# Kernel optimization log

Measured on AMD Instinct MI355X. Metric: run time of the kernel, lower is better.

Reference implementation:

```python
import jax, jax.numpy as jnp
import numpy as np

DIM = 1024
HEADS = 16
DIM_HEAD = 64
DEPTH = 12
LN_EPS = 1e-5


def setup_inputs() -> dict:
    key = jax.random.key(0)
    k1, k2, k3 = jax.random.split(key, 3)
    B, N = 4, 2048
    inner = HEADS * DIM_HEAD
    x = jax.random.normal(k1, (B, N, DIM), dtype=jnp.float32)
    ln_w = jnp.ones((DIM,), jnp.float32)
    ln_b = jnp.zeros((DIM,), jnp.float32)
    w_qkv = jax.random.normal(k2, (DIM, 3 * inner), jnp.float32) * (DIM ** -0.5)
    w_out = jax.random.normal(k3, (inner, DIM), jnp.float32) * (inner ** -0.5)
    b_out = jnp.zeros((DIM,), jnp.float32)
    return {"x": x, "ln_w": ln_w, "ln_b": ln_b, "w_qkv": w_qkv,
            "w_out": w_out, "b_out": b_out, "layer_index": 2}


def reference(x, ln_w, ln_b, w_qkv, w_out, b_out, layer_index):
    B, N, D = x.shape
    scale = DIM_HEAD ** -0.5
    # LayerNorm
    mu = jnp.mean(x, axis=-1, keepdims=True)
    var = jnp.mean(jnp.square(x - mu), axis=-1, keepdims=True)
    xn = (x - mu) * jax.lax.rsqrt(var + LN_EPS) * ln_w + ln_b
    # QKV projection (no bias), split heads: b n (h d) -> b h n d
    qkv = xn @ w_qkv  # [B, N, 3*H*Dh]
    q, k, v = jnp.split(qkv, 3, axis=-1)
    def heads(t):
        return t.reshape(B, N, HEADS, DIM_HEAD).transpose(0, 2, 1, 3)
    q, k, v = heads(q), heads(k), heads(v)
    dots = jnp.einsum('bhnd,bhmd->bhnm', q, k) * scale  # [B,H,N,N]
    if layer_index < DEPTH // 2:
        attn = jax.nn.relu(dots)
    else:
        attn = jax.nn.softmax(dots, axis=-1)
    attn = attn / N  # divide by x.shape[1]
    out = jnp.einsum('bhnm,bhmd->bhnd', attn, v)
    out = out.transpose(0, 2, 1, 3).reshape(B, N, HEADS * DIM_HEAD)
    # to_out (heads > 1): Linear + (inactive) dropout
    return out @ w_out + b_out
```

## Files before the change

### kernel.cpp

```cpp
#include <hip/hip_runtime.h>
#include <stdint.h>

typedef __bf16 bf16x8 __attribute__((ext_vector_type(8)));
typedef __bf16 bf16x4 __attribute__((ext_vector_type(4)));
typedef float f32x4 __attribute__((ext_vector_type(4)));

#define PSCALE (0.125f / 2048.0f)

#define GLOAD16(src, dst)                                                      \
  __builtin_amdgcn_global_load_lds(                                            \
      (__attribute__((address_space(1))) void*)const_cast<__bf16*>(src),       \
      (__attribute__((address_space(3))) void*)(dst), 16, 0, 0)

__global__ __launch_bounds__(256) void ln_fused(const float* __restrict__ x,
                                                const float* __restrict__ w,
                                                const float* __restrict__ b,
                                                __bf16* __restrict__ xn) {
  const int row = blockIdx.x;
  const int t = threadIdx.x;
  const float4 v = ((const float4*)(x + (size_t)row * 1024))[t];
  float s = v.x + v.y + v.z + v.w;
  float ss = v.x * v.x + v.y * v.y + v.z * v.z + v.w * v.w;
#pragma unroll
  for (int o = 32; o; o >>= 1) {
    s += __shfl_down(s, o);
    ss += __shfl_down(ss, o);
  }
  __shared__ float red[8];
  if ((t & 63) == 0) {
    red[t >> 6] = s;
    red[4 + (t >> 6)] = ss;
  }
  __syncthreads();
  const float tot = red[0] + red[1] + red[2] + red[3];
  const float tot2 = red[4] + red[5] + red[6] + red[7];
  const float mu = tot * (1.0f / 1024.0f);
  const float var = tot2 * (1.0f / 1024.0f) - mu * mu;
  const float rs = rsqrtf(var + 1e-5f);
  const float4 wv = ((const float4*)w)[t];
  const float4 bv = ((const float4*)b)[t];
  bf16x4 o;
  o[0] = (__bf16)((v.x - mu) * rs * wv.x + bv.x);
  o[1] = (__bf16)((v.y - mu) * rs * wv.y + bv.y);
  o[2] = (__bf16)((v.z - mu) * rs * wv.z + bv.z);
  o[3] = (__bf16)((v.w - mu) * rs * wv.w + bv.w);
  ((bf16x4*)xn)[(size_t)row * 256 + t] = o;
}

__global__ __launch_bounds__(256) void transpose_cvt(const float* __restrict__ A,
                                                     __bf16* __restrict__ At,
                                                     int R, int C) {
  __shared__ __bf16 T[64][72];
  const int rb = blockIdx.y * 64, cb = blockIdx.x * 64;
  const int tid = threadIdx.x;
  const int r = tid >> 2, cg = tid & 3;
#pragma unroll
  for (int k = 0; k < 4; ++k) {
    const float4 v =
        *(const float4*)(A + (size_t)(rb + r) * C + cb + cg * 16 + k * 4);
    T[cg * 16 + k * 4 + 0][r] = (__bf16)v.x;
    T[cg * 16 + k * 4 + 1][r] = (__bf16)v.y;
    T[cg * 16 + k * 4 + 2][r] = (__bf16)v.z;
    T[cg * 16 + k * 4 + 3][r] = (__bf16)v.w;
  }
  __syncthreads();
#pragma unroll
  for (int i = 0; i < 2; ++i) {
    const int j = i * 256 + tid;
    const int c = j >> 3, s8 = j & 7;
    const bf16x8 o = *(const bf16x8*)&T[c][s8 * 8];
    *(bf16x8*)(At + (size_t)(cb + c) * R + rb + s8 * 8) = o;
  }
}

__device__ __forceinline__ void stage_128x64(const __bf16* __restrict__ g,
                                             int ld, __bf16* lds) {
  const int lane = threadIdx.x & 63, w = threadIdx.x >> 6;
#pragma unroll
  for (int i = 0; i < 4; ++i) {
    const int j = i * 256 + w * 64 + lane;
    const int row = j >> 3, slot = j & 7;
    const __bf16* src = g + (size_t)row * ld + ((slot ^ (row & 7)) << 3);
    GLOAD16(src, lds + (size_t)(i * 256 + w * 64) * 8);
  }
}

template <int MODE>
__global__ __launch_bounds__(256) void gemm_nt(
    const __bf16* __restrict__ A, const __bf16* __restrict__ B, int K,
    float* __restrict__ outF, __bf16* __restrict__ Qo, __bf16* __restrict__ Ko,
    __bf16* __restrict__ Vto, const float* __restrict__ bias) {
  __shared__ __bf16 As[128 * 64];
  __shared__ __bf16 Bs[128 * 64];
  const int lane = threadIdx.x & 63, w = threadIdx.x >> 6;
  const int rb = blockIdx.y * 128, cb = blockIdx.x * 128;
  const int wr = (w >> 1) * 64, wc = (w & 1) * 64;
  f32x4 acc[4][4] = {};
  const __bf16* Ab = A + (size_t)rb * K;
  const __bf16* Bb = B + (size_t)cb * K;
  const int nkb = K >> 6;
  for (int kb = 0; kb < nkb; ++kb) {
    stage_128x64(Ab + kb * 64, K, As);
    stage_128x64(Bb + kb * 64, K, Bs);
    __syncthreads();
#pragma unroll
    for (int ks = 0; ks < 2; ++ks) {
      bf16x8 af[4], bfr[4];
      const int kc = ks * 4 + (lane >> 4);
#pragma unroll
      for (int rt = 0; rt < 4; ++rt) {
        const int lr = wr + rt * 16 + (lane & 15);
        af[rt] = *(const bf16x8*)(As + lr * 64 + ((kc ^ (lr & 7)) << 3));
      }
#pragma unroll
      for (int ct = 0; ct < 4; ++ct) {
        const int lc = wc + ct * 16 + (lane & 15);
        bfr[ct] = *(const bf16x8*)(Bs + lc * 64 + ((kc ^ (lc & 7)) << 3));
      }
#pragma unroll
      for (int rt = 0; rt < 4; ++rt)
#pragma unroll
        for (int ct = 0; ct < 4; ++ct)
          acc[rt][ct] = __builtin_amdgcn_mfma_f32_16x16x32_bf16(
              af[rt], bfr[ct], acc[rt][ct], 0, 0, 0);
    }
    __syncthreads();
  }
  const int r0 = rb + wr + (lane >> 4) * 4;
  if (MODE == 1) {
#pragma unroll
    for (int ct = 0; ct < 4; ++ct) {
      const int col = cb + wc + ct * 16 + (lane & 15);
      const float bv = bias[col];
#pragma unroll
      for (int rt = 0; rt < 4; ++rt) {
        const int row = r0 + rt * 16;
#pragma unroll
        for (int r = 0; r < 4; ++r)
          outF[(size_t)(row + r) * 1024 + col] = acc[rt][ct][r] + bv;
      }
    }
  } else {
#pragma unroll
    for (int ct = 0; ct < 4; ++ct) {
      const int col = cb + wc + ct * 16 + (lane & 15);
      const int part = col >> 10, rem = col & 1023;
      const int h = rem >> 6, d = rem & 63;
#pragma unroll
      for (int rt = 0; rt < 4; ++rt) {
        const int row = r0 + rt * 16;
        const int bi = row >> 11, n = row & 2047;
        const size_t bh = (size_t)bi * 16 + h;
        if (part == 2) {
          bf16x4 pv;
#pragma unroll
          for (int r = 0; r < 4; ++r) pv[r] = (__bf16)acc[rt][ct][r];
          *(bf16x4*)(Vto + (bh * 64 + d) * 2048 + n) = pv;
        } else if (part == 0) {
          __bf16* dst = Qo + (bh * 2048 + n) * 64 + d;
#pragma unroll
          for (int r = 0; r < 4; ++r)
            dst[(size_t)r * 64] = (__bf16)(acc[rt][ct][r] * PSCALE);
        } else {
          __bf16* dst = Ko + (bh * 2048 + n) * 64 + d;
#pragma unroll
          for (int r = 0; r < 4; ++r) dst[(size_t)r * 64] = (__bf16)acc[rt][ct][r];
        }
      }
    }
  }
}

__global__ __launch_bounds__(512) void attn_relu(
    const __bf16* __restrict__ Q, const __bf16* __restrict__ K,
    const __bf16* __restrict__ Vt, __bf16* __restrict__ O) {
  __shared__ __bf16 Ks[2][128 * 64];
  __shared__ __bf16 Vs[2][64 * 128];
  const int tid = threadIdx.x;
  const int lane = tid & 63, w = tid >> 6;
  const int g = lane >> 4, c15 = lane & 15;
  const int bh = blockIdx.x, qb = blockIdx.y;
  const __bf16* Qg = Q + ((size_t)bh * 2048 + qb * 256) * 64;
  const __bf16* Kg = K + (size_t)bh * 2048 * 64;
  const __bf16* Vg = Vt + (size_t)bh * 64 * 2048;

  const __bf16* kp0;
  const __bf16* kp1;
  const __bf16* vp0;
  const __bf16* vp1;
  {
    const int j0 = tid, j1 = 512 + tid;
    const int r0_ = j0 >> 3, s0_ = j0 & 7;
    const int r1_ = j1 >> 3, s1_ = j1 & 7;
    const int sr0 = (r0_ & 96) | ((r0_ & 12) << 1) | ((r0_ & 16) >> 2) | (r0_ & 3);
    const int sr1 = (r1_ & 96) | ((r1_ & 12) << 1) | ((r1_ & 16) >> 2) | (r1_ & 3);
    kp0 = Kg + (size_t)sr0 * 64 + ((s0_ ^ (r0_ & 7)) << 3);
    kp1 = Kg + (size_t)sr1 * 64 + ((s1_ ^ (r1_ & 7)) << 3);
    const int d0_ = j0 >> 4, t0_ = j0 & 15;
    const int d1_ = j1 >> 4, t1_ = j1 & 15;
    vp0 = Vg + (size_t)d0_ * 2048 + ((t0_ ^ (d0_ & 15)) << 3);
    vp1 = Vg + (size_t)d1_ * 2048 + ((t1_ ^ (d1_ & 15)) << 3);
  }
  const int dstoff = w * 64 * 8;

  bf16x8 qf[2][2];
#pragma unroll
  for (int rt = 0; rt < 2; ++rt)
#pragma unroll
    for (int ks = 0; ks < 2; ++ks) {
      const int row = w * 32 + rt * 16 + c15;
      qf[rt][ks] = *(const bf16x8*)(Qg + row * 64 + ks * 32 + (g << 3));
    }
  f32x4 oacc[2][4] = {};

  GLOAD16(kp0, Ks[0] + dstoff);
  GLOAD16(kp1, Ks[0] + 512 * 8 + dstoff);
  GLOAD16(vp0, Vs[0] + dstoff);
  GLOAD16(vp1, Vs[0] + 512 * 8 + dstoff);
  kp0 += 128 * 64; kp1 += 128 * 64; vp0 += 128; vp1 += 128;

  for (int kb = 0; kb < 16; ++kb) {
    const int cur = kb & 1;
    if (kb < 15) {
      GLOAD16(kp0, Ks[cur ^ 1] + dstoff);
      GLOAD16(kp1, Ks[cur ^ 1] + 512 * 8 + dstoff);
      GLOAD16(vp0, Vs[cur ^ 1] + dstoff);
      GLOAD16(vp1, Vs[cur ^ 1] + 512 * 8 + dstoff);
      kp0 += 128 * 64; kp1 += 128 * 64; vp0 += 128; vp1 += 128;
      asm volatile("s_waitcnt vmcnt(4)" ::: "memory");
    } else {
      asm volatile("s_waitcnt vmcnt(0)" ::: "memory");
    }
    __builtin_amdgcn_s_barrier();
    const __bf16* __restrict__ Kc = Ks[cur];
    const __bf16* __restrict__ Vc = Vs[cur];
#pragma unroll
    for (int u = 0; u < 4; ++u) {
      const int kra = u * 32 + c15;
      const int krb = u * 32 + 16 + c15;
      const bf16x8 kfa0 = *(const bf16x8*)(Kc + kra * 64 + ((g ^ (kra & 7)) << 3));
      const bf16x8 kfa1 = *(const bf16x8*)(Kc + kra * 64 + (((4 + g) ^ (kra & 7)) << 3));
      const bf16x8 kfb0 = *(const bf16x8*)(Kc + krb * 64 + ((g ^ (krb & 7)) << 3));
      const bf16x8 kfb1 = *(const bf16x8*)(Kc + krb * 64 + (((4 + g) ^ (krb & 7)) << 3));
      f32x4 sa[2] = {{}, {}}, sb[2] = {{}, {}};
      __builtin_amdgcn_s_setprio(1);
#pragma unroll
      for (int rt = 0; rt < 2; ++rt) {
        sa[rt] = __builtin_amdgcn_mfma_f32_16x16x32_bf16(kfa0, qf[rt][0], sa[rt], 0, 0, 0);
        sa[rt] = __builtin_amdgcn_mfma_f32_16x16x32_bf16(kfa1, qf[rt][1], sa[rt], 0, 0, 0);
        sb[rt] = __builtin_amdgcn_mfma_f32_16x16x32_bf16(kfb0, qf[rt][0], sb[rt], 0, 0, 0);
        sb[rt] = __builtin_amdgcn_mfma_f32_16x16x32_bf16(kfb1, qf[rt][1], sb[rt], 0, 0, 0);
      }
      __builtin_amdgcn_s_setprio(0);
      bf16x8 pa[2];
#pragma unroll
      for (int rt = 0; rt < 2; ++rt)
#pragma unroll
        for (int r = 0; r < 4; ++r) {
          pa[rt][r] = (__bf16)fmaxf(sa[rt][r], 0.0f);
          pa[rt][4 + r] = (__bf16)fmaxf(sb[rt][r], 0.0f);
        }
      __builtin_amdgcn_s_setprio(1);
#pragma unroll
      for (int dt = 0; dt < 4; ++dt) {
        const int d = dt * 16 + c15;
        const bf16x8 vb = *(const bf16x8*)(Vc + d * 128 + (((4 * u + g) ^ c15) << 3));
#pragma unroll
        for (int rt = 0; rt < 2; ++rt)
          oacc[rt][dt] = __builtin_amdgcn_mfma_f32_16x16x32_bf16(
              pa[rt], vb, oacc[rt][dt], 0, 0, 0);
      }
      __builtin_amdgcn_s_setprio(0);
    }
    __builtin_amdgcn_s_barrier();
  }
  const int bi = bh >> 4, h = bh & 15;
#pragma unroll
  for (int rt = 0; rt < 2; ++rt)
#pragma unroll
    for (int dt = 0; dt < 4; ++dt) {
      const int col = h * 64 + dt * 16 + c15;
      const int n0 = qb * 256 + w * 32 + rt * 16 + g * 4;
      __bf16* dst = O + ((size_t)bi * 2048 + n0) * 1024 + col;
#pragma unroll
      for (int r = 0; r < 4; ++r) dst[(size_t)r * 1024] = (__bf16)oacc[rt][dt][r];
    }
}

extern "C" void kernel_launch(void* const* d_in, const int* in_sizes, int n_in,
                              void* d_out, int out_size, void* d_ws,
                              size_t ws_size, hipStream_t stream) {
  (void)in_sizes; (void)n_in; (void)out_size; (void)ws_size;
  const float* x = (const float*)d_in[0];
  const float* ln_w = (const float*)d_in[1];
  const float* ln_b = (const float*)d_in[2];
  const float* w_qkv = (const float*)d_in[3];
  const float* w_out = (const float*)d_in[4];
  const float* b_out = (const float*)d_in[5];
  char* ws = (char*)d_ws;
  __bf16* xn = (__bf16*)(ws);
  __bf16* Wt1 = (__bf16*)(ws + (size_t)(16u << 20));
  __bf16* Wt2 = (__bf16*)(ws + (size_t)(22u << 20));
  __bf16* Qb = (__bf16*)(ws + (size_t)(24u << 20));
  __bf16* Kb = (__bf16*)(ws + (size_t)(40u << 20));
  __bf16* Vtb = (__bf16*)(ws + (size_t)(56u << 20));
  __bf16* Ob = (__bf16*)(ws + (size_t)(72u << 20));
  float* out = (float*)d_out;

  ln_fused<<<8192, 256, 0, stream>>>(x, ln_w, ln_b, xn);
  transpose_cvt<<<dim3(48, 16), 256, 0, stream>>>(w_qkv, Wt1, 1024, 3072);
  transpose_cvt<<<dim3(16, 16), 256, 0, stream>>>(w_out, Wt2, 1024, 1024);
  gemm_nt<0><<<dim3(24, 64), 256, 0, stream>>>(xn, Wt1, 1024, nullptr, Qb, Kb,
                                               Vtb, nullptr);
  attn_relu<<<dim3(64, 8), 512, 0, stream>>>(Qb, Kb, Vtb, Ob);
  gemm_nt<1><<<dim3(8, 64), 256, 0, stream>>>(Ob, Wt2, 1024, out, nullptr,
                                              nullptr, nullptr, b_out);
}
```

Baseline: 167.3 us.

## Triple-buffer GEMM staging with async LDS loads and 128x256 tiles

Reworks both projection GEMMs so each block computes a 128x256 tile with 512 threads, keeping three LDS buffers. Global-to-LDS loads run two k-steps ahead, using vmcnt waits plus a single barrier per step, and MFMA sections get raised scheduling priority. The aim is to hide global load latency and halve the syncs per k-step. In exchange it uses more LDS per block and halves the block count, which may lower occupancy and leave some CUs idle for the small output GEMM (256 blocks).

```diff
diff --git a/kernel.cpp b/kernel.cpp
--- a/kernel.cpp
+++ b/kernel.cpp
@@ -73,68 +73,99 @@
   }
 }
 
-__device__ __forceinline__ void stage_128x64(const __bf16* __restrict__ g,
-                                             int ld, __bf16* lds) {
-  const int lane = threadIdx.x & 63, w = threadIdx.x >> 6;
-#pragma unroll
-  for (int i = 0; i < 4; ++i) {
-    const int j = i * 256 + w * 64 + lane;
-    const int row = j >> 3, slot = j & 7;
-    const __bf16* src = g + (size_t)row * ld + ((slot ^ (row & 7)) << 3);
-    GLOAD16(src, lds + (size_t)(i * 256 + w * 64) * 8);
-  }
-}
-
 template <int MODE>
-__global__ __launch_bounds__(256) void gemm_nt(
+__global__ __launch_bounds__(512) void gemm_nt(
     const __bf16* __restrict__ A, const __bf16* __restrict__ B, int K,
     float* __restrict__ outF, __bf16* __restrict__ Qo, __bf16* __restrict__ Ko,
     __bf16* __restrict__ Vto, const float* __restrict__ bias) {
-  __shared__ __bf16 As[128 * 64];
-  __shared__ __bf16 Bs[128 * 64];
-  const int lane = threadIdx.x & 63, w = threadIdx.x >> 6;
-  const int rb = blockIdx.y * 128, cb = blockIdx.x * 128;
-  const int wr = (w >> 1) * 64, wc = (w & 1) * 64;
+  __shared__ __bf16 Sm[3 * 24576];
+  const int tid = threadIdx.x;
+  const int lane = tid & 63, w = tid >> 6;
+  const int g = lane >> 4, c15 = lane & 15;
+  const int wr = w >> 2, wc = w & 3;
+  const int rb = blockIdx.y * 128, cb = blockIdx.x * 256;
+
+  const __bf16* aSp[2];
+  const __bf16* bSp[4];
+  int aDo[2], bDo[4];
+#pragma unroll
+  for (int i = 0; i < 2; ++i) {
+    const int j = i * 512 + tid, row = j >> 3, slot = j & 7;
+    aSp[i] = A + (size_t)(rb + row) * K + ((slot ^ (row & 7)) << 3);
+    aDo[i] = i * 4096 + w * 512;
+  }
+#pragma unroll
+  for (int i = 0; i < 4; ++i) {
+    const int j = i * 512 + tid, col = j >> 3, slot = j & 7;
+    bSp[i] = B + (size_t)(cb + col) * K + ((slot ^ (col & 7)) << 3);
+    bDo[i] = 8192 + i * 4096 + w * 512;
+  }
+
   f32x4 acc[4][4] = {};
-  const __bf16* Ab = A + (size_t)rb * K;
-  const __bf16* Bb = B + (size_t)cb * K;
   const int nkb = K >> 6;
+
+#pragma unroll
+  for (int t = 0; t < 2; ++t) {
+    __bf16* dst = Sm + t * 24576;
+#pragma unroll
+    for (int i = 0; i < 2; ++i) GLOAD16(aSp[i] + t * 64, dst + aDo[i]);
+#pragma unroll
+    for (int i = 0; i < 4; ++i) GLOAD16(bSp[i] + t * 64, dst + bDo[i]);
+  }
+
+  int cur = 0, stg = 2, koff = 128;
   for (int kb = 0; kb < nkb; ++kb) {
-    stage_128x64(Ab + kb * 64, K, As);
-    stage_128x64(Bb + kb * 64, K, Bs);
-    __syncthreads();
+    if (kb == nkb - 1) {
+      asm volatile("s_waitcnt vmcnt(0)" ::: "memory");
+    } else {
+      asm volatile("s_waitcnt vmcnt(6)" ::: "memory");
+    }
+    __builtin_amdgcn_s_barrier();
+    if (kb < nkb - 2) {
+      __bf16* dst = Sm + stg * 24576;
+#pragma unroll
+      for (int i = 0; i < 2; ++i) GLOAD16(aSp[i] + koff, dst + aDo[i]);
+#pragma unroll
+      for (int i = 0; i < 4; ++i) GLOAD16(bSp[i] + koff, dst + bDo[i]);
+      koff += 64;
+    }
+    const __bf16* __restrict__ Ac = Sm + cur * 24576;
+    const __bf16* __restrict__ Bc = Ac + 8192;
 #pragma unroll
     for (int ks = 0; ks < 2; ++ks) {
       bf16x8 af[4], bfr[4];
-      const int kc = ks * 4 + (lane >> 4);
+      const int kc = ks * 4 + g;
 #pragma unroll
       for (int rt = 0; rt < 4; ++rt) {
-        const int lr = wr + rt * 16 + (lane & 15);
-        af[rt] = *(const bf16x8*)(As + lr * 64 + ((kc ^ (lr & 7)) << 3));
+        const int lr = wr * 64 + rt * 16 + c15;
+        af[rt] = *(const bf16x8*)(Ac + lr * 64 + ((kc ^ (lr & 7)) << 3));
       }
 #pragma unroll
       for (int ct = 0; ct < 4; ++ct) {
-        const int lc = wc + ct * 16 + (lane & 15);
-        bfr[ct] = *(const bf16x8*)(Bs + lc * 64 + ((kc ^ (lc & 7)) << 3));
-      }
+        const int lc = wc * 64 + ct * 16 + c15;
+        bfr[ct] = *(const bf16x8*)(Bc + lc * 64 + ((kc ^ (lc & 7)) << 3));
+      }
+      __builtin_amdgcn_s_setprio(1);
 #pragma unroll
       for (int rt = 0; rt < 4; ++rt)
 #pragma unroll
         for (int ct = 0; ct < 4; ++ct)
           acc[rt][ct] = __builtin_amdgcn_mfma_f32_16x16x32_bf16(
               af[rt], bfr[ct], acc[rt][ct], 0, 0, 0);
-    }
-    __syncthreads();
-  }
-  const int r0 = rb + wr + (lane >> 4) * 4;
+      __builtin_amdgcn_s_setprio(0);
+    }
+    cur = (cur == 2) ? 0 : cur + 1;
+    stg = (stg == 2) ? 0 : stg + 1;
+  }
+  const int r00 = rb + wr * 64 + g * 4;
   if (MODE == 1) {
 #pragma unroll
     for (int ct = 0; ct < 4; ++ct) {
-      const int col = cb + wc + ct * 16 + (lane & 15);
+      const int col = cb + wc * 64 + ct * 16 + c15;
       const float bv = bias[col];
 #pragma unroll
       for (int rt = 0; rt < 4; ++rt) {
-        const int row = r0 + rt * 16;
+        const int row = r00 + rt * 16;
 #pragma unroll
         for (int r = 0; r < 4; ++r)
           outF[(size_t)(row + r) * 1024 + col] = acc[rt][ct][r] + bv;
@@ -143,12 +174,12 @@
   } else {
 #pragma unroll
     for (int ct = 0; ct < 4; ++ct) {
-      const int col = cb + wc + ct * 16 + (lane & 15);
+      const int col = cb + wc * 64 + ct * 16 + c15;
       const int part = col >> 10, rem = col & 1023;
       const int h = rem >> 6, d = rem & 63;
 #pragma unroll
       for (int rt = 0; rt < 4; ++rt) {
-        const int row = r0 + rt * 16;
+        const int row = r00 + rt * 16;
         const int bi = row >> 11, n = row & 2047;
         const size_t bh = (size_t)bi * 16 + h;
         if (part == 2) {
@@ -310,9 +341,9 @@
   ln_fused<<<8192, 256, 0, stream>>>(x, ln_w, ln_b, xn);
   transpose_cvt<<<dim3(48, 16), 256, 0, stream>>>(w_qkv, Wt1, 1024, 3072);
   transpose_cvt<<<dim3(16, 16), 256, 0, stream>>>(w_out, Wt2, 1024, 1024);
-  gemm_nt<0><<<dim3(24, 64), 256, 0, stream>>>(xn, Wt1, 1024, nullptr, Qb, Kb,
+  gemm_nt<0><<<dim3(12, 64), 512, 0, stream>>>(xn, Wt1, 1024, nullptr, Qb, Kb,
                                                Vtb, nullptr);
   attn_relu<<<dim3(64, 8), 512, 0, stream>>>(Qb, Kb, Vtb, Ob);
-  gemm_nt<1><<<dim3(8, 64), 256, 0, stream>>>(Ob, Wt2, 1024, out, nullptr,
+  gemm_nt<1><<<dim3(4, 64), 512, 0, stream>>>(Ob, Wt2, 1024, out, nullptr,
                                               nullptr, nullptr, b_out);
 }
```

Measured after the change: 165.9 us. No clear change (-0.9%).
